# Optimization experiments

Measured on AMD Instinct MI355X. Metric: run time of the kernel, lower is better.

## Reference

```python
import jax, jax.numpy as jnp
import numpy as np

EPS_PRE = 1e-05   # constant added to raw scores in the torch module
EPS_NORM = 1e-12  # F.normalize default eps


def setup_inputs() -> dict:
    key = jax.random.key(0)
    kq, kk, kv = jax.random.split(key, 3)
    B, H, S, D = 2, 8, 2048, 64
    query = jax.random.normal(kq, (B, H, S, D), dtype=jnp.float32)
    keys = jax.random.normal(kk, (B, H, S, D), dtype=jnp.float32)
    vals = jax.random.normal(kv, (B, H, S, D), dtype=jnp.float32)
    # causal mask, broadcastable over batch and heads; mask==0 -> score zeroed
    mask = jnp.tril(jnp.ones((S, S), dtype=jnp.int32))[None, None, :, :]
    return {"query": query, "keys": keys, "vals": vals, "mask": mask}


def reference(query, keys, vals, mask):
    # preattn: [B,H,S,S]
    preattn = jnp.einsum("bhsd,bhtd->bhst", query, keys) + EPS_PRE
    preattn = jnp.where(mask == 0, 0.0, preattn)
    # F.normalize(dim=-1): x / max(||x||_2, eps)
    norm = jnp.sqrt(jnp.sum(preattn * preattn, axis=-1, keepdims=True))
    attn = preattn / jnp.maximum(norm, EPS_NORM)
    # dropout is identity in eval mode (reference baseline)
    out = jnp.einsum("bhst,bhtd->bhsd", attn, vals)
    return (out, attn)
```

## Files before the change

kernel.cpp:

```cpp
#include <hip/hip_runtime.h>

#define S_DIM 2048
#define D_DIM 64
#define BH    16
#define EPS_PRE  1e-5f
#define EPS_NORM 1e-12f
#define CT 8

#define WS_G   0
#define WS_M   (BH*32*4096)
#define WS_GV  (2*BH*32*4096)
#define WS_MV  (WS_GV + BH*32*64)
#define WS_RI  (WS_MV + BH*32*64)
#define FRAG_F (BH*32*2048)
#define WS_KAH (WS_RI + BH*2048)
#define WS_KAL (WS_KAH + FRAG_F)
#define WS_VAH (WS_KAL + FRAG_F)
#define WS_VAL (WS_VAH + FRAG_F)

typedef __attribute__((ext_vector_type(8))) short bf8;
typedef __attribute__((ext_vector_type(4))) float f32x4;

static __device__ __forceinline__ unsigned fbits(float x){ union{float f;unsigned u;}v; v.f=x; return v.u; }
static __device__ __forceinline__ float bcast(unsigned u){ union{unsigned u;float f;}v; v.u=u; return v.f; }

static __device__ __forceinline__ void split2(float x, unsigned short& h, unsigned short& l){
  unsigned u = fbits(x);
  h = (unsigned short)(u >> 16);
  float lo = x - bcast(u & 0xffff0000u);
  l = (unsigned short)(fbits(lo) >> 16);
}

static __device__ __forceinline__ void pack4f(float x0, float x1, float x2, float x3,
                                              uint2& hh, uint2& ll){
  unsigned u0=fbits(x0),u1=fbits(x1),u2=fbits(x2),u3=fbits(x3);
  hh.x = (u0>>16) | (u1 & 0xffff0000u);
  hh.y = (u2>>16) | (u3 & 0xffff0000u);
  float l0 = x0 - bcast(u0&0xffff0000u);
  float l1 = x1 - bcast(u1&0xffff0000u);
  float l2 = x2 - bcast(u2&0xffff0000u);
  float l3 = x3 - bcast(u3&0xffff0000u);
  ll.x = (fbits(l0)>>16) | (fbits(l1)&0xffff0000u);
  ll.y = (fbits(l2)>>16) | (fbits(l3)&0xffff0000u);
}

static __device__ __forceinline__ f32x4 mfma16(bf8 a, bf8 b, f32x4 c){
  return __builtin_amdgcn_mfma_f32_16x16x32_bf16(a, b, c, 0, 0, 0);
}

static __device__ __forceinline__ void decode(int c, int& rb, int& ck){
  int g = 0;
  while (c >= 4*(g+1)*(g+2)) ++g;
  const int off = c - 4*g*(g+1);
  const int nk = g + 1;
  const int q = off / nk;
  rb = g*8 + q;
  ck = off - q*nk;
}

__global__ __launch_bounds__(256, 4)
void lka_pack(const float* __restrict__ Kg, const float* __restrict__ Vg,
              float* __restrict__ ws)
{
  __shared__ short kHi[4096], kLo[4096];
  __shared__ short vHi[4096], vLo[4096];

  const int tid = threadIdx.x;
  const int blk = blockIdx.x;
  const int bh  = blk & 15;
  const int ti  = blk >> 4;

  const float* Kb = Kg + (size_t)bh * (S_DIM * D_DIM);
  const float* Vb = Vg + (size_t)bh * (S_DIM * D_DIM);

  {
    const int t  = tid >> 2;
    const int db = (tid & 3) * 16;
    const float* kp = Kb + (size_t)(ti*64 + t) * D_DIM + db;
    #pragma unroll
    for (int c = 0; c < 4; ++c) {
      float4 kv = *(const float4*)(kp + 4*c);
      uint2 hh, ll; pack4f(kv.x, kv.y, kv.z, kv.w, hh, ll);
      const int idx = t*64 + ((db + 4*c) ^ ((t & 7) << 3));
      *(uint2*)&kHi[idx] = hh;
      *(uint2*)&kLo[idx] = ll;
    }
  }
  {
    const int d  = (tid & 31) * 2;
    const int tb = (tid >> 5) * 8;
    float2 rr[8];
    #pragma unroll
    for (int k = 0; k < 8; ++k)
      rr[k] = *(const float2*)(Vb + (size_t)(ti*64 + tb + k) * D_DIM + d);
    #pragma unroll
    for (int dd = 0; dd < 2; ++dd) {
      union { bf8 v; unsigned short h[8]; } H, L;
      #pragma unroll
      for (int k = 0; k < 8; ++k) split2(dd ? rr[k].y : rr[k].x, H.h[k], L.h[k]);
      const int dc = d + dd;
      const int idx = dc*64 + (tb ^ ((dc & 7) << 3));
      *(bf8*)&vHi[idx] = H.v;
      *(bf8*)&vLo[idx] = L.v;
    }
  }
  __syncthreads();

  const int w = tid >> 6, ln = tid & 63, gq = ln >> 4, i16 = ln & 15;
  short* KAh = (short*)(ws + WS_KAH);
  short* KAl = (short*)(ws + WS_KAL);
  short* VAh = (short*)(ws + WS_VAH);
  short* VAl = (short*)(ws + WS_VAL);

  #pragma unroll
  for (int ff = 0; ff < 2; ++ff) {
    const int f  = w*2 + ff;
    const int ks = f >> 2, rf = f & 3;
    const int r   = rf*16 + i16;
    const int idx = r*64 + ((ks*32 + gq*8) ^ ((r & 7) << 3));
    const size_t o = ((size_t)(bh*32 + ti)*8 + f)*512 + ln*8;
    *(bf8*)(KAh + o) = *(const bf8*)&kHi[idx];
    *(bf8*)(KAl + o) = *(const bf8*)&kLo[idx];
    *(bf8*)(VAh + o) = *(const bf8*)&vHi[idx];
    *(bf8*)(VAl + o) = *(const bf8*)&vLo[idx];
  }
}

__global__ __launch_bounds__(256, 4)
void lka_gram(const float* __restrict__ Kg, float* __restrict__ ws,
              float* __restrict__ Og, float* __restrict__ Ag)
{
  __shared__ short tHi[4096], tLo[4096];

  const int tid = threadIdx.x;
  const int wv  = tid >> 6;
  const int ln  = tid & 63;
  const int gq  = ln >> 4;
  const int i16 = ln & 15;

  const int blk = blockIdx.x;
  const int bh  = blk & 15;
  const int ti  = blk >> 4;

  const float* Kb = Kg + (size_t)bh * (S_DIM * D_DIM);

  {
    f32x4 z = (f32x4){0.f,0.f,0.f,0.f};
    f32x4* p = (f32x4*)(Og + (size_t)blk * 4096);
    for (int c = tid; c < 1024; c += 256) p[c] = z;
  }
  {
    const int c0 = (ti + 1) * 64;
    const int n4 = (S_DIM - c0) >> 2;
    float* rowp = Ag + (size_t)bh * S_DIM * S_DIM + (size_t)(ti*64 + (tid>>2)) * S_DIM + c0;
    f32x4 z = (f32x4){0.f,0.f,0.f,0.f};
    for (int c = tid & 3; c < n4; c += 4)
      __builtin_nontemporal_store(z, (f32x4*)(rowp + 4*c));
  }

  {
    const int d  = (tid & 31) * 2;
    const int tb = (tid >> 5) * 8;
    float2 rr[8];
    #pragma unroll
    for (int k = 0; k < 8; ++k)
      rr[k] = *(const float2*)(Kb + (size_t)(ti*64 + tb + k) * D_DIM + d);
    #pragma unroll
    for (int dd = 0; dd < 2; ++dd) {
      union { bf8 v; unsigned short h[8]; } H, L;
      #pragma unroll
      for (int k = 0; k < 8; ++k) split2(dd ? rr[k].y : rr[k].x, H.h[k], L.h[k]);
      const int dc = d + dd;
      const int idx = dc*64 + (tb ^ ((dc & 7) << 3));
      *(bf8*)&tHi[idx] = H.v;
      *(bf8*)&tLo[idx] = L.v;
    }
  }

  float gsum = 0.f;
  if (tid < 64) {
    #pragma unroll 8
    for (int t = 0; t < 64; ++t) gsum += Kb[(size_t)(ti*64 + t) * D_DIM + tid];
  }
  __syncthreads();

  const int d2 = wv*16 + i16;
  bf8 bhi[2], blo[2];
  #pragma unroll
  for (int ks = 0; ks < 2; ++ks) {
    const int bi = d2*64 + ((ks*32 + gq*8) ^ ((d2 & 7) << 3));
    bhi[ks] = *(const bf8*)&tHi[bi];
    blo[ks] = *(const bf8*)&tLo[bi];
  }
  f32x4 acc[4];
  #pragma unroll
  for (int rf = 0; rf < 4; ++rf) acc[rf] = (f32x4){0.f,0.f,0.f,0.f};
  #pragma unroll
  for (int ks = 0; ks < 2; ++ks) {
    #pragma unroll
    for (int rf = 0; rf < 4; ++rf) {
      const int d1 = rf*16 + i16;
      const int ai = d1*64 + ((ks*32 + gq*8) ^ ((d1 & 7) << 3));
      bf8 ahi = *(const bf8*)&tHi[ai];
      bf8 alo = *(const bf8*)&tLo[ai];
      acc[rf] = mfma16(ahi, bhi[ks], acc[rf]);
      acc[rf] = mfma16(alo, bhi[ks], acc[rf]);
      acc[rf] = mfma16(ahi, blo[ks], acc[rf]);
    }
  }
  float* Gp = ws + WS_G + (size_t)(bh*32 + ti) * 4096;
  #pragma unroll
  for (int rf = 0; rf < 4; ++rf)
    *(f32x4*)(Gp + d2*64 + rf*16 + gq*4) = acc[rf];

  if (tid < 64) ws[WS_GV + (size_t)(bh*32 + ti)*64 + tid] = gsum;
}

__global__ __launch_bounds__(256, 8)
void lka_prefix(float* __restrict__ ws)
{
  const int tid = threadIdx.x;
  const int blk = blockIdx.x;
  const int bh  = blk >> 2;
  const int r4  = blk & 3;

  const int row = r4*16 + (tid >> 4);
  const int c4  = (tid & 15) * 4;

  const float* Gp = ws + WS_G + (size_t)(bh*32)*4096 + row*64 + c4;
  float*       Mp = ws + WS_M + (size_t)(bh*32)*4096 + row*64 + c4;

  f32x4 acc = (f32x4){0.f,0.f,0.f,0.f};
  #pragma unroll 4
  for (int i = 0; i < 32; ++i) {
    *(f32x4*)(Mp + (size_t)i*4096) = acc;
    f32x4 g = *(const f32x4*)(Gp + (size_t)i*4096);
    acc[0]+=g[0]; acc[1]+=g[1]; acc[2]+=g[2]; acc[3]+=g[3];
  }

  if (r4 == 0 && tid < 64) {
    float a = 0.f;
    #pragma unroll 4
    for (int i = 0; i < 32; ++i) {
      ws[WS_MV + (size_t)(bh*32 + i)*64 + tid] = a;
      a += ws[WS_GV + (size_t)(bh*32 + i)*64 + tid];
    }
  }
}

__global__ __launch_bounds__(256, 4)
void lka_rownorm(const float* __restrict__ Qg, const float* __restrict__ Kg,
                 float* __restrict__ ws)
{
  __shared__ short kHi[4096], kLo[4096];
  __shared__ short mHi[4096], mLo[4096];
  __shared__ float mvS[64];

  const int tid = threadIdx.x;
  const int wv  = tid >> 6;
  const int ln  = tid & 63;
  const int gq  = ln >> 4;
  const int i16 = ln & 15;

  const int blk = blockIdx.x;
  const int bh  = blk & 15;
  const int rb  = blk >> 4;
  const int s0  = rb * 64;

  const float* Qb = Qg + (size_t)bh * (S_DIM * D_DIM);
  const float* Kb = Kg + (size_t)bh * (S_DIM * D_DIM);

  const int srow = s0 + wv*16 + i16;

  {
    const int r  = tid >> 2;
    const int db = (tid & 3) * 16;
    const float* kp = Kb + (size_t)(s0 + r) * D_DIM + db;
    const float* mp = ws + WS_M + (size_t)(bh*32 + rb)*4096 + r*64 + db;
    #pragma unroll
    for (int c = 0; c < 4; ++c) {
      float4 kv = *(const float4*)(kp + 4*c);
      uint2 hh, ll; pack4f(kv.x, kv.y, kv.z, kv.w, hh, ll);
      const int idx = r*64 + ((db + 4*c) ^ ((r & 7) << 3));
      *(uint2*)&kHi[idx] = hh;
      *(uint2*)&kLo[idx] = ll;
      float4 mv = *(const float4*)(mp + 4*c);
      uint2 mh, mlo; pack4f(mv.x, mv.y, mv.z, mv.w, mh, mlo);
      *(uint2*)&mHi[idx] = mh;
      *(uint2*)&mLo[idx] = mlo;
    }
  }
  if (tid < 64) mvS[tid] = ws[WS_MV + (size_t)(bh*32 + rb)*64 + tid];

  bf8 qhi[2], qlo[2];
  #pragma unroll
  for (int ks = 0; ks < 2; ++ks) {
    const float* qp = Qb + (size_t)srow * D_DIM + ks*32 + gq*8;
    float4 a = *(const float4*)qp;
    float4 b = *(const float4*)(qp + 4);
    union { bf8 v; unsigned short h[8]; } H, L;
    float f0[8] = {a.x,a.y,a.z,a.w,b.x,b.y,b.z,b.w};
    #pragma unroll
    for (int j = 0; j < 8; ++j) split2(f0[j], H.h[j], L.h[j]);
    qhi[ks] = H.v; qlo[ks] = L.v;
  }
  __syncthreads();

  f32x4 accS[4], accY[4];
  #pragma unroll
  for (int rf = 0; rf < 4; ++rf) { accS[rf] = (f32x4){0.f,0.f,0.f,0.f}; accY[rf] = (f32x4){0.f,0.f,0.f,0.f}; }
  #pragma unroll
  for (int ks = 0; ks < 2; ++ks) {
    #pragma unroll
    for (int rf = 0; rf < 4; ++rf) {
      const int r   = rf*16 + i16;
      const int idx = r*64 + ((ks*32 + gq*8) ^ ((r & 7) << 3));
      bf8 ahi = *(const bf8*)&kHi[idx];
      bf8 alo = *(const bf8*)&kLo[idx];
      accS[rf] = mfma16(ahi, qhi[ks], accS[rf]);
      accS[rf] = mfma16(alo, qhi[ks], accS[rf]);
      accS[rf] = mfma16(ahi, qlo[ks], accS[rf]);
      bf8 Ahi = *(const bf8*)&mHi[idx];
      bf8 Alo = *(const bf8*)&mLo[idx];
      accY[rf] = mfma16(Ahi, qhi[ks], accY[rf]);
      accY[rf] = mfma16(Alo, qhi[ks], accY[rf]);
      accY[rf] = mfma16(Ahi, qlo[ks], accY[rf]);
    }
  }

  float ssq = 0.f;
  #pragma unroll
  for (int rf = 0; rf < 4; ++rf) {
    f32x4 q4 = *(const f32x4*)(Qb + (size_t)srow * D_DIM + rf*16 + gq*4);
    f32x4 m4 = *(const f32x4*)&mvS[rf*16 + gq*4];
    #pragma unroll
    for (int rg = 0; rg < 4; ++rg) {
      ssq += q4[rg] * (accY[rf][rg] + 2.f*EPS_PRE*m4[rg]);
      const int t = s0 + rf*16 + gq*4 + rg;
      if (t <= srow) { const float x = accS[rf][rg] + EPS_PRE; ssq += x*x; }
    }
  }
  ssq += __shfl_xor(ssq, 16);
  ssq += __shfl_xor(ssq, 32);
  ssq += EPS_PRE*EPS_PRE * (float)(rb*64);
  ssq = fmaxf(ssq, 0.f);
  const float rinv = 1.f / fmaxf(sqrtf(ssq), EPS_NORM);
  if (gq == 0) ws[WS_RI + (size_t)bh*S_DIM + srow] = rinv;
}

__global__ __launch_bounds__(256, 4)
void lka_emit(const float* __restrict__ Qg, const float* __restrict__ ws,
              float* __restrict__ Og, float* __restrict__ Ag)
{
  __shared__ short pHi[4096], pLo[4096];

  const int tid = threadIdx.x;
  const int wv  = tid >> 6;
  const int ln  = tid & 63;
  const int gq  = ln >> 4;
  const int i16 = ln & 15;

  const int blk = blockIdx.x;
  const int bh  = blk & 15;
  int rb, ck; decode(blk >> 4, rb, ck);
  const int s0 = rb * 64;

  const float* Qb = Qg + (size_t)bh * (S_DIM * D_DIM);
  float* Ob = Og + (size_t)bh * (S_DIM * D_DIM);
  float* Ab = Ag + (size_t)bh * ((size_t)S_DIM * S_DIM);

  const int srow = s0 + wv*16 + i16;

  const float rinv = ws[WS_RI + (size_t)bh*S_DIM + srow];

  const short* KAh = (const short*)(ws + WS_KAH);
  const short* KAl = (const short*)(ws + WS_KAL);
  const short* VAh = (const short*)(ws + WS_VAH);
  const short* VAl = (const short*)(ws + WS_VAL);

  bf8 qhi[2], qlo[2];
  #pragma unroll
  for (int ks = 0; ks < 2; ++ks) {
    const float* qp = Qb + (size_t)srow * D_DIM + ks*32 + gq*8;
    float4 a = *(const float4*)qp;
    float4 b = *(const float4*)(qp + 4);
    union { bf8 v; unsigned short h[8]; } H, L;
    float f0[8] = {a.x,a.y,a.z,a.w,b.x,b.y,b.z,b.w};
    #pragma unroll
    for (int j = 0; j < 8; ++j) split2(f0[j], H.h[j], L.h[j]);
    qhi[ks] = H.v; qlo[ks] = L.v;
  }

  f32x4 oacc[4];
  #pragma unroll
  for (int rf = 0; rf < 4; ++rf) oacc[rf] = (f32x4){0.f,0.f,0.f,0.f};

  const int pR = wv*16 + i16;

  const int j0 = ck * CT;
  const int j1 = min(j0 + CT, rb + 1);
  for (int j = j0; j < j1; ++j) {
    const size_t tb = ((size_t)(bh*32 + j)*8)*512 + ln*8;

    f32x4 acc[4];
    #pragma unroll
    for (int rf = 0; rf < 4; ++rf) acc[rf] = (f32x4){0.f,0.f,0.f,0.f};
    #pragma unroll
    for (int ks = 0; ks < 2; ++ks) {
      #pragma unroll
      for (int rf = 0; rf < 4; ++rf) {
        const size_t o = tb + (size_t)(ks*4 + rf)*512;
        bf8 ahi = *(const bf8*)(KAh + o);
        bf8 alo = *(const bf8*)(KAl + o);
        acc[rf] = mfma16(ahi, qhi[ks], acc[rf]);
        acc[rf] = mfma16(alo, qhi[ks], acc[rf]);
        acc[rf] = mfma16(ahi, qlo[ks], acc[rf]);
      }
    }

    #pragma unroll
    for (int rf = 0; rf < 4; ++rf) {
      f32x4 x;
      #pragma unroll
      for (int rg = 0; rg < 4; ++rg) {
        const int t = j*64 + rf*16 + gq*4 + rg;
        float v = acc[rf][rg] + EPS_PRE;
        if (j == rb && t > srow) v = 0.f;
        x[rg] = v * rinv;
      }
      __builtin_nontemporal_store(x, (f32x4*)(Ab + (size_t)srow * S_DIM + j*64 + rf*16 + gq*4));
      uint2 hh, ll; pack4f(x[0], x[1], x[2], x[3], hh, ll);
      const int pidx = pR*64 + ((rf*16 + gq*4) ^ ((pR & 7) << 3));
      *(uint2*)&pHi[pidx] = hh;
      *(uint2*)&pLo[pidx] = ll;
    }

    #pragma unroll
    for (int ks = 0; ks < 2; ++ks) {
      const int pi = pR*64 + ((ks*32 + gq*8) ^ ((pR & 7) << 3));
      bf8 bhi = *(const bf8*)&pHi[pi];
      bf8 blo = *(const bf8*)&pLo[pi];
      #pragma unroll
      for (int rfd = 0; rfd < 4; ++rfd) {
        const size_t o = tb + (size_t)(ks*4 + rfd)*512;
        bf8 ahi = *(const bf8*)(VAh + o);
        bf8 alo = *(const bf8*)(VAl + o);
        oacc[rfd] = mfma16(ahi, bhi, oacc[rfd]);
        oacc[rfd] = mfma16(alo, bhi, oacc[rfd]);
        oacc[rfd] = mfma16(ahi, blo, oacc[rfd]);
      }
    }
  }

  #pragma unroll
  for (int rfd = 0; rfd < 4; ++rfd)
    #pragma unroll
    for (int rg = 0; rg < 4; ++rg)
      atomicAdd(&Ob[(size_t)srow * D_DIM + rfd*16 + gq*4 + rg], oacc[rfd][rg]);
}

extern "C" void kernel_launch(void* const* d_in, const int* in_sizes, int n_in,
                              void* d_out, int out_size, void* d_ws, size_t ws_size,
                              hipStream_t stream) {
  (void)in_sizes; (void)n_in; (void)out_size; (void)ws_size;
  const float* Q = (const float*)d_in[0];
  const float* K = (const float*)d_in[1];
  const float* V = (const float*)d_in[2];
  float* out  = (float*)d_out;
  float* attn = out + (size_t)BH * S_DIM * D_DIM;
  float* ws   = (float*)d_ws;

  lka_pack   <<<dim3(512),  dim3(256), 0, stream>>>(K, V, ws);
  lka_gram   <<<dim3(512),  dim3(256), 0, stream>>>(K, ws, out, attn);
  lka_prefix <<<dim3(64),   dim3(256), 0, stream>>>(ws);
  lka_rownorm<<<dim3(512),  dim3(256), 0, stream>>>(Q, K, ws);
  lka_emit   <<<dim3(BH*80),dim3(256), 0, stream>>>(Q, ws, out, attn);
}
```

Before: 437.6 us.

## Compute output via prefix K^T V matrices instead of per-tile PV in emit

Result: faster. 404.3 us (-7.6%).

```diff
diff --git a/kernel.cpp b/kernel.cpp
--- a/kernel.cpp
+++ b/kernel.cpp
@@ -7,16 +7,19 @@
 #define EPS_NORM 1e-12f
 #define CT 8
 
+#define TILE_F 4096
+#define FRAG_F (BH*32*2048)
 #define WS_G   0
-#define WS_M   (BH*32*4096)
-#define WS_GV  (2*BH*32*4096)
-#define WS_MV  (WS_GV + BH*32*64)
-#define WS_RI  (WS_MV + BH*32*64)
-#define FRAG_F (BH*32*2048)
+#define WS_W   (WS_G  + BH*32*TILE_F)
+#define WS_M   (WS_W  + BH*32*TILE_F)
+#define WS_WP  (WS_M  + BH*32*TILE_F)
+#define WS_GV  (WS_WP + BH*32*TILE_F)
+#define WS_VV  (WS_GV + BH*32*64)
+#define WS_MV  (WS_VV + BH*32*64)
+#define WS_UV  (WS_MV + BH*32*64)
+#define WS_RI  (WS_UV + BH*32*64)
 #define WS_KAH (WS_RI + BH*2048)
 #define WS_KAL (WS_KAH + FRAG_F)
-#define WS_VAH (WS_KAL + FRAG_F)
-#define WS_VAL (WS_VAH + FRAG_F)
 
 typedef __attribute__((ext_vector_type(8))) short bf8;
 typedef __attribute__((ext_vector_type(4))) float f32x4;
@@ -58,79 +61,13 @@
   ck = off - q*nk;
 }
 
-__global__ __launch_bounds__(256, 4)
-void lka_pack(const float* __restrict__ Kg, const float* __restrict__ Vg,
-              float* __restrict__ ws)
+__global__ __launch_bounds__(256, 3)
+void lka_prep(const float* __restrict__ Kg, const float* __restrict__ Vg,
+              float* __restrict__ ws, float* __restrict__ Ag)
 {
-  __shared__ short kHi[4096], kLo[4096];
-  __shared__ short vHi[4096], vLo[4096];
-
-  const int tid = threadIdx.x;
-  const int blk = blockIdx.x;
-  const int bh  = blk & 15;
-  const int ti  = blk >> 4;
-
-  const float* Kb = Kg + (size_t)bh * (S_DIM * D_DIM);
-  const float* Vb = Vg + (size_t)bh * (S_DIM * D_DIM);
-
-  {
-    const int t  = tid >> 2;
-    const int db = (tid & 3) * 16;
-    const float* kp = Kb + (size_t)(ti*64 + t) * D_DIM + db;
-    #pragma unroll
-    for (int c = 0; c < 4; ++c) {
-      float4 kv = *(const float4*)(kp + 4*c);
-      uint2 hh, ll; pack4f(kv.x, kv.y, kv.z, kv.w, hh, ll);
-      const int idx = t*64 + ((db + 4*c) ^ ((t & 7) << 3));
-      *(uint2*)&kHi[idx] = hh;
-      *(uint2*)&kLo[idx] = ll;
-    }
-  }
-  {
-    const int d  = (tid & 31) * 2;
-    const int tb = (tid >> 5) * 8;
-    float2 rr[8];
-    #pragma unroll
-    for (int k = 0; k < 8; ++k)
-      rr[k] = *(const float2*)(Vb + (size_t)(ti*64 + tb + k) * D_DIM + d);
-    #pragma unroll
-    for (int dd = 0; dd < 2; ++dd) {
-      union { bf8 v; unsigned short h[8]; } H, L;
-      #pragma unroll
-      for (int k = 0; k < 8; ++k) split2(dd ? rr[k].y : rr[k].x, H.h[k], L.h[k]);
-      const int dc = d + dd;
-      const int idx = dc*64 + (tb ^ ((dc & 7) << 3));
-      *(bf8*)&vHi[idx] = H.v;
-      *(bf8*)&vLo[idx] = L.v;
-    }
-  }
-  __syncthreads();
-
-  const int w = tid >> 6, ln = tid & 63, gq = ln >> 4, i16 = ln & 15;
-  short* KAh = (short*)(ws + WS_KAH);
-  short* KAl = (short*)(ws + WS_KAL);
-  short* VAh = (short*)(ws + WS_VAH);
-  short* VAl = (short*)(ws + WS_VAL);
-
-  #pragma unroll
-  for (int ff = 0; ff < 2; ++ff) {
-    const int f  = w*2 + ff;
-    const int ks = f >> 2, rf = f & 3;
-    const int r   = rf*16 + i16;
-    const int idx = r*64 + ((ks*32 + gq*8) ^ ((r & 7) << 3));
-    const size_t o = ((size_t)(bh*32 + ti)*8 + f)*512 + ln*8;
-    *(bf8*)(KAh + o) = *(const bf8*)&kHi[idx];
-    *(bf8*)(KAl + o) = *(const bf8*)&kLo[idx];
-    *(bf8*)(VAh + o) = *(const bf8*)&vHi[idx];
-    *(bf8*)(VAl + o) = *(const bf8*)&vLo[idx];
-  }
-}
-
-__global__ __launch_bounds__(256, 4)
-void lka_gram(const float* __restrict__ Kg, float* __restrict__ ws,
-              float* __restrict__ Og, float* __restrict__ Ag)
-{
-  __shared__ short tHi[4096], tLo[4096];
+  __shared__ short kTh[4096], kTl[4096];
+  __shared__ short vTh[4096], vTl[4096];
+  __shared__ short kRh[4096], kRl[4096];
 
   const int tid = threadIdx.x;
   const int wv  = tid >> 6;
@@ -143,12 +80,8 @@
   const int ti  = blk >> 4;
 
   const float* Kb = Kg + (size_t)bh * (S_DIM * D_DIM);
-
-  {
-    f32x4 z = (f32x4){0.f,0.f,0.f,0.f};
-    f32x4* p = (f32x4*)(Og + (size_t)blk * 4096);
-    for (int c = tid; c < 1024; c += 256) p[c] = z;
-  }
+  const float* Vb = Vg + (size_t)bh * (S_DIM * D_DIM);
+
   {
     const int c0 = (ti + 1) * 64;
     const int n4 = (S_DIM - c0) >> 2;
@@ -161,10 +94,184 @@
   {
     const int d  = (tid & 31) * 2;
     const int tb = (tid >> 5) * 8;
+    float2 kr[8], vr[8];
+    #pragma unroll
+    for (int k = 0; k < 8; ++k) {
+      kr[k] = *(const float2*)(Kb + (size_t)(ti*64 + tb + k) * D_DIM + d);
+      vr[k] = *(const float2*)(Vb + (size_t)(ti*64 + tb + k) * D_DIM + d);
+    }
+    #pragma unroll
+    for (int dd = 0; dd < 2; ++dd) {
+      union { bf8 v; unsigned short h[8]; } KH, KL, VH, VL;
+      #pragma unroll
+      for (int k = 0; k < 8; ++k) {
+        split2(dd ? kr[k].y : kr[k].x, KH.h[k], KL.h[k]);
+        split2(dd ? vr[k].y : vr[k].x, VH.h[k], VL.h[k]);
+      }
+      const int dc = d + dd;
+      const int idx = dc*64 + (tb ^ ((dc & 7) << 3));
+      *(bf8*)&kTh[idx] = KH.v; *(bf8*)&kTl[idx] = KL.v;
+      *(bf8*)&vTh[idx] = VH.v; *(bf8*)&vTl[idx] = VL.v;
+    }
+  }
+  {
+    const int t  = tid >> 2;
+    const int db = (tid & 3) * 16;
+    const float* kp = Kb + (size_t)(ti*64 + t) * D_DIM + db;
+    #pragma unroll
+    for (int c = 0; c < 4; ++c) {
+      float4 kv = *(const float4*)(kp + 4*c);
+      uint2 hh, ll; pack4f(kv.x, kv.y, kv.z, kv.w, hh, ll);
+      const int idx = t*64 + ((db + 4*c) ^ ((t & 7) << 3));
+      *(uint2*)&kRh[idx] = hh;
+      *(uint2*)&kRl[idx] = ll;
+    }
+  }
+  float gsum = 0.f, vsum = 0.f;
+  if (tid < 64) {
+    #pragma unroll 8
+    for (int t = 0; t < 64; ++t) {
+      gsum += Kb[(size_t)(ti*64 + t) * D_DIM + tid];
+      vsum += Vb[(size_t)(ti*64 + t) * D_DIM + tid];
+    }
+  }
+  __syncthreads();
+
+  const int d2 = wv*16 + i16;
+  bf8 bkh[2], bkl[2], bvh[2], bvl[2];
+  #pragma unroll
+  for (int ks = 0; ks < 2; ++ks) {
+    const int bi = d2*64 + ((ks*32 + gq*8) ^ ((d2 & 7) << 3));
+    bkh[ks] = *(const bf8*)&kTh[bi]; bkl[ks] = *(const bf8*)&kTl[bi];
+    bvh[ks] = *(const bf8*)&vTh[bi]; bvl[ks] = *(const bf8*)&vTl[bi];
+  }
+  f32x4 accG[4], accW[4];
+  #pragma unroll
+  for (int rf = 0; rf < 4; ++rf) { accG[rf]=(f32x4){0,0,0,0}; accW[rf]=(f32x4){0,0,0,0}; }
+  #pragma unroll
+  for (int ks = 0; ks < 2; ++ks) {
+    #pragma unroll
+    for (int rf = 0; rf < 4; ++rf) {
+      const int d1 = rf*16 + i16;
+      const int ai = d1*64 + ((ks*32 + gq*8) ^ ((d1 & 7) << 3));
+      bf8 ahi = *(const bf8*)&kTh[ai];
+      bf8 alo = *(const bf8*)&kTl[ai];
+      accG[rf] = mfma16(ahi, bkh[ks], accG[rf]);
+      accG[rf] = mfma16(alo, bkh[ks], accG[rf]);
+      accG[rf] = mfma16(ahi, bkl[ks], accG[rf]);
+      accW[rf] = mfma16(ahi, bvh[ks], accW[rf]);
+      accW[rf] = mfma16(alo, bvh[ks], accW[rf]);
+      accW[rf] = mfma16(ahi, bvl[ks], accW[rf]);
+    }
+  }
+  float* Gp = ws + WS_G + (size_t)(bh*32 + ti) * TILE_F;
+  float* Wp = ws + WS_W + (size_t)(bh*32 + ti) * TILE_F;
+  #pragma unroll
+  for (int rf = 0; rf < 4; ++rf) {
+    *(f32x4*)(Gp + d2*64 + rf*16 + gq*4) = accG[rf];
+    *(f32x4*)(Wp + d2*64 + rf*16 + gq*4) = accW[rf];
+  }
+  if (tid < 64) {
+    ws[WS_GV + (size_t)(bh*32 + ti)*64 + tid] = gsum;
+    ws[WS_VV + (size_t)(bh*32 + ti)*64 + tid] = vsum;
+  }
+
+  short* KAh = (short*)(ws + WS_KAH);
+  short* KAl = (short*)(ws + WS_KAL);
+  #pragma unroll
+  for (int ff = 0; ff < 2; ++ff) {
+    const int f  = wv*2 + ff;
+    const int ks = f >> 2, rf = f & 3;
+    const int r   = rf*16 + i16;
+    const int idx = r*64 + ((ks*32 + gq*8) ^ ((r & 7) << 3));
+    const size_t o = ((size_t)(bh*32 + ti)*8 + f)*512 + ln*8;
+    *(bf8*)(KAh + o) = *(const bf8*)&kRh[idx];
+    *(bf8*)(KAl + o) = *(const bf8*)&kRl[idx];
+  }
+}
+
+__global__ __launch_bounds__(256, 8)
+void lka_prefix(float* __restrict__ ws)
+{
+  const int tid = threadIdx.x;
+  const int blk = blockIdx.x;
+  const int bh  = blk >> 3;
+  const int sel = (blk >> 2) & 1;
+  const int r4  = blk & 3;
+
+  const int row = r4*16 + (tid >> 4);
+  const int c4  = (tid & 15) * 4;
+
+  const float* Sp = ws + (sel ? WS_W : WS_G) + (size_t)(bh*32)*TILE_F + row*64 + c4;
+  float*       Dp = ws + (sel ? WS_WP : WS_M) + (size_t)(bh*32)*TILE_F + row*64 + c4;
+
+  f32x4 acc = (f32x4){0.f,0.f,0.f,0.f};
+  #pragma unroll 4
+  for (int i = 0; i < 32; ++i) {
+    *(f32x4*)(Dp + (size_t)i*TILE_F) = acc;
+    f32x4 g = *(const f32x4*)(Sp + (size_t)i*TILE_F);
+    acc[0]+=g[0]; acc[1]+=g[1]; acc[2]+=g[2]; acc[3]+=g[3];
+  }
+
+  if (r4 == 0 && tid < 64) {
+    const int so = sel ? WS_VV : WS_GV;
+    const int doo = sel ? WS_UV : WS_MV;
+    float a = 0.f;
+    #pragma unroll 4
+    for (int i = 0; i < 32; ++i) {
+      ws[doo + (size_t)(bh*32 + i)*64 + tid] = a;
+      a += ws[so + (size_t)(bh*32 + i)*64 + tid];
+    }
+  }
+}
+
+__global__ __launch_bounds__(256, 3)
+void lka_rno(const float* __restrict__ Qg, const float* __restrict__ Vg,
+             float* __restrict__ ws, float* __restrict__ Og)
+{
+  __shared__ short aH[4096], aL[4096];
+  __shared__ short vTh[4096], vTl[4096];
+  __shared__ short pH[4096], pL[4096];
+  __shared__ float mvS[64], uvS[64];
+
+  const int tid = threadIdx.x;
+  const int wv  = tid >> 6;
+  const int ln  = tid & 63;
+  const int gq  = ln >> 4;
+  const int i16 = ln & 15;
+
+  const int blk = blockIdx.x;
+  const int bh  = blk & 15;
+  const int rb  = blk >> 4;
+  const int s0  = rb * 64;
+
+  const float* Qb = Qg + (size_t)bh * (S_DIM * D_DIM);
+  const float* Vb = Vg + (size_t)bh * (S_DIM * D_DIM);
+  float* Ob = Og + (size_t)bh * (S_DIM * D_DIM);
+
+  const int srow = s0 + wv*16 + i16;
+  const int pR   = wv*16 + i16;
+
+  {
+    const int r  = tid >> 2;
+    const int db = (tid & 3) * 16;
+    const float* mp = ws + WS_M + (size_t)(bh*32 + rb)*TILE_F + r*64 + db;
+    #pragma unroll
+    for (int c = 0; c < 4; ++c) {
+      float4 mv = *(const float4*)(mp + 4*c);
+      uint2 hh, ll; pack4f(mv.x, mv.y, mv.z, mv.w, hh, ll);
+      const int idx = r*64 + ((db + 4*c) ^ ((r & 7) << 3));
+      *(uint2*)&aH[idx] = hh;
+      *(uint2*)&aL[idx] = ll;
+    }
+  }
+  {
+    const int d  = (tid & 31) * 2;
+    const int tb = (tid >> 5) * 8;
     float2 rr[8];
     #pragma unroll
     for (int k = 0; k < 8; ++k)
-      rr[k] = *(const float2*)(Kb + (size_t)(ti*64 + tb + k) * D_DIM + d);
+      rr[k] = *(const float2*)(Vb + (size_t)(s0 + tb + k) * D_DIM + d);
     #pragma unroll
     for (int dd = 0; dd < 2; ++dd) {
       union { bf8 v; unsigned short h[8]; } H, L;
@@ -172,125 +279,14 @@
       for (int k = 0; k < 8; ++k) split2(dd ? rr[k].y : rr[k].x, H.h[k], L.h[k]);
       const int dc = d + dd;
       const int idx = dc*64 + (tb ^ ((dc & 7) << 3));
-      *(bf8*)&tHi[idx] = H.v;
-      *(bf8*)&tLo[idx] = L.v;
-    }
-  }
-
-  float gsum = 0.f;
+      *(bf8*)&vTh[idx] = H.v;
+      *(bf8*)&vTl[idx] = L.v;
+    }
+  }
   if (tid < 64) {
-    #pragma unroll 8
-    for (int t = 0; t < 64; ++t) gsum += Kb[(size_t)(ti*64 + t) * D_DIM + tid];
-  }
-  __syncthreads();
-
-  const int d2 = wv*16 + i16;
-  bf8 bhi[2], blo[2];
-  #pragma unroll
-  for (int ks = 0; ks < 2; ++ks) {
-    const int bi = d2*64 + ((ks*32 + gq*8) ^ ((d2 & 7) << 3));
-    bhi[ks] = *(const bf8*)&tHi[bi];
-    blo[ks] = *(const bf8*)&tLo[bi];
-  }
-  f32x4 acc[4];
-  #pragma unroll
-  for (int rf = 0; rf < 4; ++rf) acc[rf] = (f32x4){0.f,0.f,0.f,0.f};
-  #pragma unroll
-  for (int ks = 0; ks < 2; ++ks) {
-    #pragma unroll
-    for (int rf = 0; rf < 4; ++rf) {
-      const int d1 = rf*16 + i16;
-      const int ai = d1*64 + ((ks*32 + gq*8) ^ ((d1 & 7) << 3));
-      bf8 ahi = *(const bf8*)&tHi[ai];
-      bf8 alo = *(const bf8*)&tLo[ai];
-      acc[rf] = mfma16(ahi, bhi[ks], acc[rf]);
-      acc[rf] = mfma16(alo, bhi[ks], acc[rf]);
-      acc[rf] = mfma16(ahi, blo[ks], acc[rf]);
-    }
-  }
-  float* Gp = ws + WS_G + (size_t)(bh*32 + ti) * 4096;
-  #pragma unroll
-  for (int rf = 0; rf < 4; ++rf)
-    *(f32x4*)(Gp + d2*64 + rf*16 + gq*4) = acc[rf];
-
-  if (tid < 64) ws[WS_GV + (size_t)(bh*32 + ti)*64 + tid] = gsum;
-}
-
-__global__ __launch_bounds__(256, 8)
-void lka_prefix(float* __restrict__ ws)
-{
-  const int tid = threadIdx.x;
-  const int blk = blockIdx.x;
-  const int bh  = blk >> 2;
-  const int r4  = blk & 3;
-
-  const int row = r4*16 + (tid >> 4);
-  const int c4  = (tid & 15) * 4;
-
-  const float* Gp = ws + WS_G + (size_t)(bh*32)*4096 + row*64 + c4;
-  float*       Mp = ws + WS_M + (size_t)(bh*32)*4096 + row*64 + c4;
-
-  f32x4 acc = (f32x4){0.f,0.f,0.f,0.f};
-  #pragma unroll 4
-  for (int i = 0; i < 32; ++i) {
-    *(f32x4*)(Mp + (size_t)i*4096) = acc;
-    f32x4 g = *(const f32x4*)(Gp + (size_t)i*4096);
-    acc[0]+=g[0]; acc[1]+=g[1]; acc[2]+=g[2]; acc[3]+=g[3];
-  }
-
-  if (r4 == 0 && tid < 64) {
-    float a = 0.f;
-    #pragma unroll 4
-    for (int i = 0; i < 32; ++i) {
-      ws[WS_MV + (size_t)(bh*32 + i)*64 + tid] = a;
-      a += ws[WS_GV + (size_t)(bh*32 + i)*64 + tid];
-    }
-  }
-}
-
-__global__ __launch_bounds__(256, 4)
-void lka_rownorm(const float* __restrict__ Qg, const float* __restrict__ Kg,
-                 float* __restrict__ ws)
-{
-  __shared__ short kHi[4096], kLo[4096];
-  __shared__ short mHi[4096], mLo[4096];
-  __shared__ float mvS[64];
-
-  const int tid = threadIdx.x;
-  const int wv  = tid >> 6;
-  const int ln  = tid & 63;
-  const int gq  = ln >> 4;
-  const int i16 = ln & 15;
-
-  const int blk = blockIdx.x;
-  const int bh  = blk & 15;
-  const int rb  = blk >> 4;
-  const int s0  = rb * 64;
-
-  const float* Qb = Qg + (size_t)bh * (S_DIM * D_DIM);
-  const float* Kb = Kg + (size_t)bh * (S_DIM * D_DIM);
-
-  const int srow = s0 + wv*16 + i16;
-
-  {
-    const int r  = tid >> 2;
-    const int db = (tid & 3) * 16;
-    const float* kp = Kb + (size_t)(s0 + r) * D_DIM + db;
-    const float* mp = ws + WS_M + (size_t)(bh*32 + rb)*4096 + r*64 + db;
-    #pragma unroll
-    for (int c = 0; c < 4; ++c) {
-      float4 kv = *(const float4*)(kp + 4*c);
-      uint2 hh, ll; pack4f(kv.x, kv.y, kv.z, kv.w, hh, ll);
-      const int idx = r*64 + ((db + 4*c) ^ ((r & 7) << 3));
-      *(uint2*)&kHi[idx] = hh;
-      *(uint2*)&kLo[idx] = ll;
-      float4 mv = *(const float4*)(mp + 4*c);
-      uint2 mh, mlo; pack4f(mv.x, mv.y, mv.z, mv.w, mh, mlo);
-      *(uint2*)&mHi[idx] = mh;
-      *(uint2*)&mLo[idx] = mlo;
-    }
-  }
-  if (tid < 64) mvS[tid] = ws[WS_MV + (size_t)(bh*32 + rb)*64 + tid];
+    mvS[tid] = ws[WS_MV + (size_t)(bh*32 + rb)*64 + tid];
+    uvS[tid] = ws[WS_UV + (size_t)(bh*32 + rb)*64 + tid];
+  }
 
   bf8 qhi[2], qlo[2];
   #pragma unroll
@@ -304,27 +300,31 @@
     for (int j = 0; j < 8; ++j) split2(f0[j], H.h[j], L.h[j]);
     qhi[ks] = H.v; qlo[ks] = L.v;
   }
+  const short* KAh = (const short*)(ws + WS_KAH);
+  const short* KAl = (const short*)(ws + WS_KAL);
+  const size_t tb0 = ((size_t)(bh*32 + rb)*8)*512 + ln*8;
   __syncthreads();
 
   f32x4 accS[4], accY[4];
   #pragma unroll
-  for (int rf = 0; rf < 4; ++rf) { accS[rf] = (f32x4){0.f,0.f,0.f,0.f}; accY[rf] = (f32x4){0.f,0.f,0.f,0.f}; }
+  for (int rf = 0; rf < 4; ++rf) { accS[rf]=(f32x4){0,0,0,0}; accY[rf]=(f32x4){0,0,0,0}; }
   #pragma unroll
   for (int ks = 0; ks < 2; ++ks) {
     #pragma unroll
     for (int rf = 0; rf < 4; ++rf) {
+      const size_t o = tb0 + (size_t)(ks*4 + rf)*512;
+      bf8 khi = *(const bf8*)(KAh + o);
+      bf8 klo = *(const bf8*)(KAl + o);
+      accS[rf] = mfma16(khi, qhi[ks], accS[rf]);
+      accS[rf] = mfma16(klo, qhi[ks], accS[rf]);
+      accS[rf] = mfma16(khi, qlo[ks], accS[rf]);
       const int r   = rf*16 + i16;
       const int idx = r*64 + ((ks*32 + gq*8) ^ ((r & 7) << 3));
-      bf8 ahi = *(const bf8*)&kHi[idx];
-      bf8 alo = *(const bf8*)&kLo[idx];
-      accS[rf] = mfma16(ahi, qhi[ks], accS[rf]);
-      accS[rf] = mfma16(alo, qhi[ks], accS[rf]);
-      accS[rf] = mfma16(ahi, qlo[ks], accS[rf]);
-      bf8 Ahi = *(const bf8*)&mHi[idx];
-      bf8 Alo = *(const bf8*)&mLo[idx];
-      accY[rf] = mfma16(Ahi, qhi[ks], accY[rf]);
-      accY[rf] = mfma16(Alo, qhi[ks], accY[rf]);
-      accY[rf] = mfma16(Ahi, qlo[ks], accY[rf]);
+      bf8 mhi = *(const bf8*)&aH[idx];
+      bf8 mlo = *(const bf8*)&aL[idx];
+      accY[rf] = mfma16(mhi, qhi[ks], accY[rf]);
+      accY[rf] = mfma16(mlo, qhi[ks], accY[rf]);
+      accY[rf] = mfma16(mhi, qlo[ks], accY[rf]);
     }
   }
 
@@ -333,12 +333,19 @@
   for (int rf = 0; rf < 4; ++rf) {
     f32x4 q4 = *(const f32x4*)(Qb + (size_t)srow * D_DIM + rf*16 + gq*4);
     f32x4 m4 = *(const f32x4*)&mvS[rf*16 + gq*4];
+    f32x4 x;
     #pragma unroll
     for (int rg = 0; rg < 4; ++rg) {
       ssq += q4[rg] * (accY[rf][rg] + 2.f*EPS_PRE*m4[rg]);
       const int t = s0 + rf*16 + gq*4 + rg;
-      if (t <= srow) { const float x = accS[rf][rg] + EPS_PRE; ssq += x*x; }
-    }
+      float v = (t <= srow) ? (accS[rf][rg] + EPS_PRE) : 0.f;
+      ssq += v * v;
+      x[rg] = v;
+    }
+    uint2 hh, ll; pack4f(x[0], x[1], x[2], x[3], hh, ll);
+    const int pidx = pR*64 + ((rf*16 + gq*4) ^ ((pR & 7) << 3));
+    *(uint2*)&pH[pidx] = hh;
+    *(uint2*)&pL[pidx] = ll;
   }
   ssq += __shfl_xor(ssq, 16);
   ssq += __shfl_xor(ssq, 32);
@@ -346,14 +353,62 @@
   ssq = fmaxf(ssq, 0.f);
   const float rinv = 1.f / fmaxf(sqrtf(ssq), EPS_NORM);
   if (gq == 0) ws[WS_RI + (size_t)bh*S_DIM + srow] = rinv;
+
+  __syncthreads();
+  {
+    const int r  = tid >> 2;
+    const int db = (tid & 3) * 16;
+    const float* wp = ws + WS_WP + (size_t)(bh*32 + rb)*TILE_F + r*64 + db;
+    #pragma unroll
+    for (int c = 0; c < 4; ++c) {
+      float4 wv4 = *(const float4*)(wp + 4*c);
+      uint2 hh, ll; pack4f(wv4.x, wv4.y, wv4.z, wv4.w, hh, ll);
+      const int idx = r*64 + ((db + 4*c) ^ ((r & 7) << 3));
+      *(uint2*)&aH[idx] = hh;
+      *(uint2*)&aL[idx] = ll;
+    }
+  }
+  __syncthreads();
+
+  f32x4 accO[4];
+  #pragma unroll
+  for (int rf = 0; rf < 4; ++rf) accO[rf]=(f32x4){0,0,0,0};
+  #pragma unroll
+  for (int ks = 0; ks < 2; ++ks) {
+    const int pi = pR*64 + ((ks*32 + gq*8) ^ ((pR & 7) << 3));
+    bf8 bph = *(const bf8*)&pH[pi];
+    bf8 bpl = *(const bf8*)&pL[pi];
+    #pragma unroll
+    for (int rf = 0; rf < 4; ++rf) {
+      const int r   = rf*16 + i16;
+      const int idx = r*64 + ((ks*32 + gq*8) ^ ((r & 7) << 3));
+      bf8 whi = *(const bf8*)&aH[idx];
+      bf8 wlo = *(const bf8*)&aL[idx];
+      accO[rf] = mfma16(whi, qhi[ks], accO[rf]);
+      accO[rf] = mfma16(wlo, qhi[ks], accO[rf]);
+      accO[rf] = mfma16(whi, qlo[ks], accO[rf]);
+      bf8 vhi = *(const bf8*)&vTh[idx];
+      bf8 vlo = *(const bf8*)&vTl[idx];
+      accO[rf] = mfma16(vhi, bph, accO[rf]);
+      accO[rf] = mfma16(vlo, bph, accO[rf]);
+      accO[rf] = mfma16(vhi, bpl, accO[rf]);
+    }
+  }
+  #pragma unroll
+  for (int rf = 0; rf < 4; ++rf) {
+    f32x4 u4 = *(const f32x4*)&uvS[rf*16 + gq*4];
+    f32x4 o4;
+    #pragma unroll
+    for (int rg = 0; rg < 4; ++rg)
+      o4[rg] = rinv * (accO[rf][rg] + EPS_PRE * u4[rg]);
+    *(f32x4*)(Ob + (size_t)srow * D_DIM + rf*16 + gq*4) = o4;
+  }
 }
 
 __global__ __launch_bounds__(256, 4)
 void lka_emit(const float* __restrict__ Qg, const float* __restrict__ ws,
-              float* __restrict__ Og, float* __restrict__ Ag)
+              float* __restrict__ Ag)
 {
-  __shared__ short pHi[4096], pLo[4096];
-
   const int tid = threadIdx.x;
   const int wv  = tid >> 6;
   const int ln  = tid & 63;
@@ -366,17 +421,13 @@
   const int s0 = rb * 64;
 
   const float* Qb = Qg + (size_t)bh * (S_DIM * D_DIM);
-  float* Ob = Og + (size_t)bh * (S_DIM * D_DIM);
   float* Ab = Ag + (size_t)bh * ((size_t)S_DIM * S_DIM);
 
   const int srow = s0 + wv*16 + i16;
-
   const float rinv = ws[WS_RI + (size_t)bh*S_DIM + srow];
 
   const short* KAh = (const short*)(ws + WS_KAH);
   const short* KAl = (const short*)(ws + WS_KAL);
-  const short* VAh = (const short*)(ws + WS_VAH);
-  const short* VAl = (const short*)(ws + WS_VAL);
 
   bf8 qhi[2], qlo[2];
   #pragma unroll
@@ -391,14 +442,11 @@
     qhi[ks] = H.v; qlo[ks] = L.v;
   }
 
-  f32x4 oacc[4];
-  #pragma unroll
-  for (int rf = 0; rf < 4; ++rf) oacc[rf] = (f32x4){0.f,0.f,0.f,0.f};
-
-  const int pR = wv*16 + i16;
+  float* Arow = Ab + (size_t)srow * S_DIM + gq*4;
 
   const int j0 = ck * CT;
   const int j1 = min(j0 + CT, rb + 1);
+  #pragma unroll 2
   for (int j = j0; j < j1; ++j) {
     const size_t tb = ((size_t)(bh*32 + j)*8)*512 + ln*8;
 
@@ -418,45 +466,28 @@
       }
     }
 
-    #pragma unroll
-    for (int rf = 0; rf < 4; ++rf) {
-      f32x4 x;
+    if (j == rb) {
       #pragma unroll
-      for (int rg = 0; rg < 4; ++rg) {
-        const int t = j*64 + rf*16 + gq*4 + rg;
-        float v = acc[rf][rg] + EPS_PRE;
-        if (j == rb && t > srow) v = 0.f;
-        x[rg] = v * rinv;
+      for (int rf = 0; rf < 4; ++rf) {
+        f32x4 x;
+        #pragma unroll
+        for (int rg = 0; rg < 4; ++rg) {
+          const int t = j*64 + rf*16 + gq*4 + rg;
+          x[rg] = (t <= srow) ? (acc[rf][rg] + EPS_PRE) * rinv : 0.f;
+        }
+        __builtin_nontemporal_store(x, (f32x4*)(Arow + j*64 + rf*16));
       }
-      __builtin_nontemporal_store(x, (f32x4*)(Ab + (size_t)srow * S_DIM + j*64 + rf*16 + gq*4));
-      uint2 hh, ll; pack4f(x[0], x[1], x[2], x[3], hh, ll);
-      const int pidx = pR*64 + ((rf*16 + gq*4) ^ ((pR & 7) << 3));
-      *(uint2*)&pHi[pidx] = hh;
-      *(uint2*)&pLo[pidx] = ll;
-    }
-
-    #pragma unroll
-    for (int ks = 0; ks < 2; ++ks) {
-      const int pi = pR*64 + ((ks*32 + gq*8) ^ ((pR & 7) << 3));
-      bf8 bhi = *(const bf8*)&pHi[pi];
-      bf8 blo = *(const bf8*)&pLo[pi];
+    } else {
       #pragma unroll
-      for (int rfd = 0; rfd < 4; ++rfd) {
-        const size_t o = tb + (size_t)(ks*4 + rfd)*512;
-        bf8 ahi = *(const bf8*)(VAh + o);
-        bf8 alo = *(const bf8*)(VAl + o);
-        oacc[rfd] = mfma16(ahi, bhi, oacc[rfd]);
-        oacc[rfd] = mfma16(alo, bhi, oacc[rfd]);
-        oacc[rfd] = mfma16(ahi, blo, oacc[rfd]);
+      for (int rf = 0; rf < 4; ++rf) {
+        f32x4 x;
+        #pragma unroll
+        for (int rg = 0; rg < 4; ++rg)
+          x[rg] = (acc[rf][rg] + EPS_PRE) * rinv;
+        __builtin_nontemporal_store(x, (f32x4*)(Arow + j*64 + rf*16));
       }
     }
   }
-
-  #pragma unroll
-  for (int rfd = 0; rfd < 4; ++rfd)
-    #pragma unroll
-    for (int rg = 0; rg < 4; ++rg)
-      atomicAdd(&Ob[(size_t)srow * D_DIM + rfd*16 + gq*4 + rg], oacc[rfd][rg]);
 }
 
 extern "C" void kernel_launch(void* const* d_in, const int* in_sizes, int n_in,
@@ -470,9 +501,8 @@
   float* attn = out + (size_t)BH * S_DIM * D_DIM;
   float* ws   = (float*)d_ws;
 
-  lka_pack   <<<dim3(512),  dim3(256), 0, stream>>>(K, V, ws);
-  lka_gram   <<<dim3(512),  dim3(256), 0, stream>>>(K, ws, out, attn);
-  lka_prefix <<<dim3(64),   dim3(256), 0, stream>>>(ws);
-  lka_rownorm<<<dim3(512),  dim3(256), 0, stream>>>(Q, K, ws);
-  lka_emit   <<<dim3(BH*80),dim3(256), 0, stream>>>(Q, ws, out, attn);
-}
+  lka_prep  <<<dim3(512),   dim3(256), 0, stream>>>(K, V, ws, attn);
+  lka_prefix<<<dim3(128),   dim3(256), 0, stream>>>(ws);
+  lka_rno   <<<dim3(512),   dim3(256), 0, stream>>>(Q, V, ws, out);
+  lka_emit  <<<dim3(BH*80), dim3(256), 0, stream>>>(Q, ws, attn);
+}
```
